# Kernel optimization log

Measured on AMD Instinct MI355X. Metric: run time of the kernel, lower is better.

## Reference

```python
import jax, jax.numpy as jnp
import numpy as np
import math

D_MODEL = 1024
N_HEADS = 16
D_HEAD = D_MODEL // N_HEADS


def setup_inputs() -> dict:
    key = jax.random.key(0)
    k_x, k_wqkv, k_bqkv, k_wp, k_bp = jax.random.split(key, 5)
    B, T = 2, 2048
    s = 1.0 / math.sqrt(D_MODEL)
    return {
        "x": jax.random.normal(k_x, (B, T, D_MODEL), dtype=jnp.float32),
        "W_qkv": jax.random.uniform(k_wqkv, (D_MODEL, 3 * D_MODEL), minval=-s, maxval=s, dtype=jnp.float32),
        "b_qkv": jax.random.uniform(k_bqkv, (3 * D_MODEL,), minval=-s, maxval=s, dtype=jnp.float32),
        "W_proj": jax.random.uniform(k_wp, (D_MODEL, D_MODEL), minval=-s, maxval=s, dtype=jnp.float32),
        "b_proj": jax.random.uniform(k_bp, (D_MODEL,), minval=-s, maxval=s, dtype=jnp.float32),
    }


def reference(x, W_qkv, b_qkv, W_proj, b_proj):
    B, T, C = x.shape
    qkv = x @ W_qkv + b_qkv                      # [B,T,3C]
    qkv = qkv.reshape(B, T, 3, N_HEADS, D_HEAD)
    qkv = jnp.transpose(qkv, (2, 0, 3, 1, 4))     # [3,B,H,T,dh]
    q, k, v = qkv[0], qkv[1], qkv[2]
    scale = math.sqrt(D_HEAD)
    attn = jnp.einsum('bhqd,bhkd->bhqk', q, k) / scale  # [B,H,T,T]
    causal = jnp.tril(jnp.ones((T, T), dtype=bool))
    attn = jnp.where(causal, attn, -jnp.inf)
    attn = jax.nn.softmax(attn, axis=-1)
    out = jnp.einsum('bhqk,bhkd->bhqd', attn, v)  # [B,H,T,dh]
    out = jnp.transpose(out, (0, 2, 1, 3)).reshape(B, T, C)
    return out @ W_proj + b_proj
```

## Files before the change

### kernel.cpp

```cpp
#include <hip/hip_runtime.h>

#define B_    2
#define T_    2048
#define C_    1024
#define H_    16
#define DH_   64
#define M_    (B_ * T_)
#define NQKV  (3 * C_)

typedef __bf16 bf16;
typedef __bf16 bf16x2 __attribute__((ext_vector_type(2)));
typedef __bf16 bf16x4 __attribute__((ext_vector_type(4)));
typedef __bf16 bf16x8 __attribute__((ext_vector_type(8)));
typedef float  f32x4  __attribute__((ext_vector_type(4)));
typedef float  f32x16 __attribute__((ext_vector_type(16)));
typedef unsigned u32x4 __attribute__((ext_vector_type(4)));

__device__ __forceinline__ void async16(const void* g, void* l) {
  __builtin_amdgcn_global_load_lds(
      (const __attribute__((address_space(1))) void*)g,
      (__attribute__((address_space(3))) void*)l, 16, 0, 0);
}

__device__ __forceinline__ unsigned pk(float a, float b) {
  bf16x2 t; t[0] = (bf16)a; t[1] = (bf16)b;
  return __builtin_bit_cast(unsigned, t);
}

__global__ __launch_bounds__(256) void prep_k(
    const float* __restrict__ x, bf16* __restrict__ xbf,
    const float* __restrict__ Wqkv, bf16* __restrict__ wqkvT,
    const float* __restrict__ Wproj, bf16* __restrict__ wprojT) {
  __shared__ float tile[32][33];
  const int bid = blockIdx.x;
  if (bid < 4096) {
    const int i = (bid * 256 + threadIdx.x) * 4;
    float4 v = *(const float4*)(x + i);
    bf16x4 o;
    o[0] = (bf16)v.x; o[1] = (bf16)v.y; o[2] = (bf16)v.z; o[3] = (bf16)v.w;
    *(bf16x4*)(xbf + i) = o;
    return;
  }
  const float* in; bf16* out; int R, C, cb, rb;
  if (bid < 4096 + 3072) {
    const int b = bid - 4096;
    in = Wqkv; out = wqkvT; R = 1024; C = 3072; cb = b % 96; rb = b / 96;
  } else {
    const int b = bid - 7168;
    in = Wproj; out = wprojT; R = 1024; C = 1024; cb = b & 31; rb = b >> 5;
  }
  const int c0 = cb * 32, r0 = rb * 32;
  const int tx = threadIdx.x & 31, ty = threadIdx.x >> 5;
#pragma unroll
  for (int j = 0; j < 4; j++)
    tile[ty + j * 8][tx] = in[(size_t)(r0 + ty + j * 8) * C + c0 + tx];
  __syncthreads();
#pragma unroll
  for (int j = 0; j < 4; j++)
    out[(size_t)(c0 + ty + j * 8) * R + r0 + tx] = (bf16)tile[tx][ty + j * 8];
}

template <int EPI, int BM, int BN>
__global__ __launch_bounds__(256) void gemm_k(
    const bf16* __restrict__ A, const bf16* __restrict__ Bt,
    const float* __restrict__ bias, float* __restrict__ outF,
    bf16* __restrict__ qb, bf16* __restrict__ kb, bf16* __restrict__ vtb) {
  constexpr int K = 1024;
  constexpr int MI = BM / 32;
  constexpr int NJ = BN / 32;
  __shared__ alignas(16) bf16 As[BM * 64];
  __shared__ alignas(16) bf16 Bs[BN * 64];
  const int tid = threadIdx.x;
  const int lane = tid & 63, wv = tid >> 6;
  const int l15 = lane & 15, quad = lane >> 4;
  const int wm = (wv >> 1) * (BM / 2), wn = (wv & 1) * (BN / 2);
  const int m0 = blockIdx.x * BM, n0 = blockIdx.y * BN;

  f32x4 acc[MI][NJ] = {};

  const int srow = tid >> 3;
  const int sgb = ((tid & 7) ^ (srow & 7)) * 8;
  const bf16* ga = A + (size_t)(m0 + srow) * K + sgb;
  const bf16* gb = Bt + (size_t)(n0 + srow) * K + sgb;
  const int swz = l15 & 7;

  for (int it = 0; it < K / 64; ++it) {
    const int k0 = it * 64;
#pragma unroll
    for (int c = 0; c < BM / 32; c++)
      async16(ga + k0 + (size_t)(c * 32) * K, As + tid * 8 + c * 2048);
#pragma unroll
    for (int c = 0; c < BN / 32; c++)
      async16(gb + k0 + (size_t)(c * 32) * K, Bs + tid * 8 + c * 2048);
    __syncthreads();
    bf16x8 af[2][MI], bfr[2][NJ];
#pragma unroll
    for (int kk = 0; kk < 2; kk++) {
#pragma unroll
      for (int i = 0; i < MI; i++)
        af[kk][i] = *(const bf16x8*)(As + (wm + i * 16 + l15) * 64 +
                                     (((kk * 4 + quad) ^ swz) << 3));
#pragma unroll
      for (int j = 0; j < NJ; j++)
        bfr[kk][j] = *(const bf16x8*)(Bs + (wn + j * 16 + l15) * 64 +
                                      (((kk * 4 + quad) ^ swz) << 3));
    }
#pragma unroll
    for (int kk = 0; kk < 2; kk++)
#pragma unroll
      for (int i = 0; i < MI; i++)
#pragma unroll
        for (int j = 0; j < NJ; j++)
          acc[i][j] = __builtin_amdgcn_mfma_f32_16x16x32_bf16(
              af[kk][i], bfr[kk][j], acc[i][j], 0, 0, 0);
    __syncthreads();
  }

#pragma unroll
  for (int i = 0; i < MI; i++) {
#pragma unroll
    for (int j = 0; j < NJ; j++) {
      const int gcol = n0 + wn + j * 16 + l15;
      const float bv = bias[gcol];
      const int trow = m0 + wm + i * 16 + quad * 4;
      if constexpr (EPI == 0) {
        const int which = gcol >> 10;
        const int hn = gcol & 1023;
        const int h = hn >> 6, d = hn & 63;
        const int bb = trow >> 11, t = trow & 2047;
        const int head = bb * 16 + h;
        if (which == 0) {
#pragma unroll
          for (int r = 0; r < 4; r++)
            qb[head * 131072 + (t + r) * 64 + d] =
                (bf16)((acc[i][j][r] + bv) * 0.1803368801f);
        } else if (which == 1) {
#pragma unroll
          for (int r = 0; r < 4; r++)
            kb[head * 131072 + (t + r) * 64 + d] = (bf16)(acc[i][j][r] + bv);
        } else {
          bf16x4 pv;
#pragma unroll
          for (int r = 0; r < 4; r++) pv[r] = (bf16)(acc[i][j][r] + bv);
          *(bf16x4*)(vtb + head * 131072 + d * 2048 + t) = pv;
        }
      } else {
#pragma unroll
        for (int r = 0; r < 4; r++)
          outF[(size_t)(trow + r) * 1024 + gcol] = acc[i][j][r] + bv;
      }
    }
  }
}

__global__ __launch_bounds__(512, 4) void attn_k(const bf16* __restrict__ Q,
                                                 const bf16* __restrict__ K,
                                                 const bf16* __restrict__ Vt,
                                                 bf16* __restrict__ O) {
  __shared__ alignas(16) bf16 Ks[2][128 * 64];
  __shared__ alignas(16) bf16 Vs[2][64 * 128];
  const int tid = threadIdx.x, lane = tid & 63, wv = tid >> 6;
  const int l31 = lane & 31, hi = lane >> 5;
  const int qs = wv & 3, halfw = wv >> 2;

  const int b = blockIdx.x;
  const int sH = b >> 8, i = b & 255;
  const int bh = (i & 7) | (((i >> 3) & 3) << 3);
  const int x = i >> 5;
  const int qJ = sH ? (15 - x) : x;
  const int q0 = qJ * 128;
  const int nIter = qJ + 1;

  const bf16* Qb = Q + (size_t)bh * 131072;
  const bf16* Kb = K + (size_t)bh * 131072;
  const bf16* Vb = Vt + (size_t)bh * 131072;

  const int krow = tid >> 3;
  const int kg = (tid & 7) ^ (krow & 7);
  const bf16* gk = Kb + krow * 64 + kg * 8;
  const int vrow = tid >> 4;
  const int vg = (tid & 15) ^ (vrow & 15);
  const bf16* gv = Vb + vrow * 2048 + vg * 8;

  const int swzk = l31 & 7;
  const int swzv = l31 & 15;
  const int bb = bh >> 4, h = bh & 15;

  const int q = q0 + qs * 32 + l31;
  bf16x8 aq[4];
#pragma unroll
  for (int ds = 0; ds < 4; ds++)
    aq[ds] = *(const bf16x8*)(Qb + q * 64 + ds * 16 + hi * 8);

  f32x16 o0 = {}, o1 = {};
  float m = -3.0e38f, lsum = 0.f;

#pragma unroll
  for (int c = 0; c < 2; c++) {
    async16(gk + c * (64 * 64), &Ks[0][tid * 8 + c * 4096]);
    async16(gv + c * (32 * 2048), &Vs[0][tid * 8 + c * 4096]);
  }

  for (int it = 0; it < nIter; ++it) {
    const int cur = it & 1;
    __syncthreads();
    if (it + 1 < nIter) {
      const int kt1 = (it + 1) * 128;
#pragma unroll
      for (int c = 0; c < 2; c++) {
        async16(gk + kt1 * 64 + c * (64 * 64), &Ks[cur ^ 1][tid * 8 + c * 4096]);
        async16(gv + kt1 + c * (32 * 2048), &Vs[cur ^ 1][tid * 8 + c * 4096]);
      }
    }
    const bf16* Kc = Ks[cur];
    const bf16* Vc = Vs[cur];

    f32x16 s[2] = {};
    __builtin_amdgcn_s_setprio(1);
#pragma unroll
    for (int nf = 0; nf < 2; nf++) {
      const int row = halfw * 64 + nf * 32 + l31;
#pragma unroll
      for (int ds = 0; ds < 4; ds++) {
        bf16x8 kf = *(const bf16x8*)(Kc + row * 64 + (((ds * 2 + hi) ^ swzk) << 3));
        s[nf] = __builtin_amdgcn_mfma_f32_32x32x16_bf16(kf, aq[ds], s[nf], 0, 0, 0);
      }
    }
    __builtin_amdgcn_s_setprio(0);

    if (it == nIter - 1) {
#pragma unroll
      for (int nf = 0; nf < 2; nf++)
#pragma unroll
        for (int r = 0; r < 16; r++) {
          const int kt = it * 128 + halfw * 64 + nf * 32 +
                         (r & 3) + 8 * (r >> 2) + 4 * hi;
          if (kt > q) s[nf][r] = -3.0e38f;
        }
    }

    float red[8];
#pragma unroll
    for (int r = 0; r < 8; r++)
      red[r] = fmaxf(fmaxf(s[0][r], s[0][r + 8]), fmaxf(s[1][r], s[1][r + 8]));
#pragma unroll
    for (int st = 4; st >= 1; st >>= 1)
#pragma unroll
      for (int r = 0; r < 4; r++)
        if (r < st) red[r] = fmaxf(red[r], red[r + st]);
    float mx = red[0];
    mx = fmaxf(mx, __shfl_xor(mx, 32));
    if (!__all(mx - m <= 8.0f)) {
      const float mnew = fmaxf(m, mx);
      const float alpha = __builtin_amdgcn_exp2f(m - mnew);
      m = mnew; lsum *= alpha;
#pragma unroll
      for (int r = 0; r < 16; r++) { o0[r] *= alpha; o1[r] *= alpha; }
    }
    float tsp[4] = {0.f, 0.f, 0.f, 0.f};
    unsigned w[2][8];
#pragma unroll
    for (int nf = 0; nf < 2; nf++)
#pragma unroll
      for (int k = 0; k < 8; k++) {
        const float pa = __builtin_amdgcn_exp2f(s[nf][2 * k] - m);
        const float pc = __builtin_amdgcn_exp2f(s[nf][2 * k + 1] - m);
        tsp[k & 3] += pa + pc;
        w[nf][k] = pk(pa, pc);
      }
    float ts = (tsp[0] + tsp[1]) + (tsp[2] + tsp[3]);
    ts += __shfl_xor(ts, 32);
    lsum += ts;

    __builtin_amdgcn_s_setprio(1);
#pragma unroll
    for (int nf = 0; nf < 2; nf++) {
#pragma unroll
      for (int hh = 0; hh < 2; hh++) {
        const unsigned w0 = w[nf][hh * 4 + 0], w1 = w[nf][hh * 4 + 1];
        const unsigned w2 = w[nf][hh * 4 + 2], w3 = w[nf][hh * 4 + 3];
        const unsigned rx = (unsigned)__shfl_xor((int)(hi ? w0 : w2), 32);
        const unsigned ry = (unsigned)__shfl_xor((int)(hi ? w1 : w3), 32);
        u32x4 pw;
        pw[0] = hi ? rx : w0;
        pw[1] = hi ? ry : w1;
        pw[2] = hi ? w2 : rx;
        pw[3] = hi ? w3 : ry;
        const bf16x8 pb = __builtin_bit_cast(bf16x8, pw);
        const int c = halfw * 4 + nf * 2 + hh;
        const bf16x8 vf0 = *(const bf16x8*)(Vc + l31 * 128 +
                                            (((c * 2 + hi) ^ swzv) << 3));
        o0 = __builtin_amdgcn_mfma_f32_32x32x16_bf16(vf0, pb, o0, 0, 0, 0);
        const bf16x8 vf1 = *(const bf16x8*)(Vc + (32 + l31) * 128 +
                                            (((c * 2 + hi) ^ swzv) << 3));
        o1 = __builtin_amdgcn_mfma_f32_32x32x16_bf16(vf1, pb, o1, 0, 0, 0);
      }
    }
    __builtin_amdgcn_s_setprio(0);
  }

  __syncthreads();
  float* oX = (float*)Vs;
  float* mX = (float*)Ks;
  const int slot = qs * 64 + lane;
  if (halfw == 1) {
#pragma unroll
    for (int r = 0; r < 16; r++) {
      oX[r * 256 + slot] = o0[r];
      oX[(16 + r) * 256 + slot] = o1[r];
    }
    mX[slot] = m;
    mX[256 + slot] = lsum;
  }
  __syncthreads();
  if (halfw == 0) {
    const float mB = mX[slot], lB = mX[256 + slot];
    const float m12 = fmaxf(m, mB);
    const float aA = __builtin_amdgcn_exp2f(m - m12);
    const float aB = __builtin_amdgcn_exp2f(mB - m12);
    const float inv = 1.0f / (lsum * aA + lB * aB);
    bf16* Op = O + (size_t)(bb * 2048 + q) * 1024 + h * 64;
#pragma unroll
    for (int g = 0; g < 4; g++) {
      bf16x4 v0, v1;
#pragma unroll
      for (int k2 = 0; k2 < 4; k2++) {
        const int r = g * 4 + k2;
        v0[k2] = (bf16)((o0[r] * aA + oX[r * 256 + slot] * aB) * inv);
        v1[k2] = (bf16)((o1[r] * aA + oX[(16 + r) * 256 + slot] * aB) * inv);
      }
      *(bf16x4*)(Op + g * 8 + hi * 4) = v0;
      *(bf16x4*)(Op + 32 + g * 8 + hi * 4) = v1;
    }
  }
}

extern "C" void kernel_launch(void* const* d_in, const int* in_sizes, int n_in,
                              void* d_out, int out_size, void* d_ws, size_t ws_size,
                              hipStream_t stream) {
  const float* x     = (const float*)d_in[0];
  const float* Wqkv  = (const float*)d_in[1];
  const float* bqkv  = (const float*)d_in[2];
  const float* Wproj = (const float*)d_in[3];
  const float* bproj = (const float*)d_in[4];
  float* out = (float*)d_out;

  char* p = (char*)d_ws;
  bf16* xbf    = (bf16*)p; p += (size_t)M_ * C_ * 2;
  bf16* wqkvT  = (bf16*)p; p += (size_t)NQKV * C_ * 2;
  bf16* wprojT = (bf16*)p; p += (size_t)C_ * C_ * 2;
  bf16* Qb     = (bf16*)p; p += (size_t)M_ * C_ * 2;
  bf16* Kb     = (bf16*)p; p += (size_t)M_ * C_ * 2;
  bf16* Vtb    = (bf16*)p; p += (size_t)M_ * C_ * 2;
  bf16* AO     = (bf16*)p;

  prep_k<<<8192, 256, 0, stream>>>(x, xbf, Wqkv, wqkvT, Wproj, wprojT);

  gemm_k<0, 128, 128><<<dim3(M_ / 128, NQKV / 128), 256, 0, stream>>>(
      xbf, wqkvT, bqkv, nullptr, Qb, Kb, Vtb);

  attn_k<<<512, 512, 0, stream>>>(Qb, Kb, Vtb, AO);

  gemm_k<1, 64, 64><<<dim3(M_ / 64, C_ / 64), 256, 0, stream>>>(
      AO, wprojT, bproj, out, nullptr, nullptr, nullptr);
}
```

Before: 165.8 us.

## Split attention key tiles across four waves with smaller query blocks

The attention kernel now handles 64-query blocks, giving twice as many workgroups. Each of 4 wave groups processes a 32-key slice of each 128-key tile, and the partial softmax states are merged by a two-level LDS tree reduction at the end. K is single-buffered with an extra barrier per iteration, and Q is reloaded from global memory each iteration instead of held in registers. The launch bound moves to 6 to raise occupancy, at the cost of more barriers, repeated Q loads and a longer cross-wave merge.

```diff
diff --git a/kernel.cpp b/kernel.cpp
--- a/kernel.cpp
+++ b/kernel.cpp
@@ -153,23 +153,23 @@
   }
 }
 
-__global__ __launch_bounds__(512, 4) void attn_k(const bf16* __restrict__ Q,
+__global__ __launch_bounds__(512, 6) void attn_k(const bf16* __restrict__ Q,
                                                  const bf16* __restrict__ K,
                                                  const bf16* __restrict__ Vt,
                                                  bf16* __restrict__ O) {
-  __shared__ alignas(16) bf16 Ks[2][128 * 64];
+  __shared__ alignas(16) bf16 Ks[128 * 64];
   __shared__ alignas(16) bf16 Vs[2][64 * 128];
   const int tid = threadIdx.x, lane = tid & 63, wv = tid >> 6;
   const int l31 = lane & 31, hi = lane >> 5;
-  const int qs = wv & 3, halfw = wv >> 2;
+  const int qs = wv & 1, ktq = wv >> 1;
 
   const int b = blockIdx.x;
-  const int sH = b >> 8, i = b & 255;
+  const int sH = b >> 9, i = b & 511;
   const int bh = (i & 7) | (((i >> 3) & 3) << 3);
   const int x = i >> 5;
-  const int qJ = sH ? (15 - x) : x;
-  const int q0 = qJ * 128;
-  const int nIter = qJ + 1;
+  const int qJ = sH ? (31 - x) : x;
+  const int q0 = qJ * 64;
+  const int nIter = (qJ >> 1) + 1;
 
   const bf16* Qb = Q + (size_t)bh * 131072;
   const bf16* Kb = K + (size_t)bh * 131072;
@@ -187,68 +187,58 @@
   const int bb = bh >> 4, h = bh & 15;
 
   const int q = q0 + qs * 32 + l31;
-  bf16x8 aq[4];
-#pragma unroll
-  for (int ds = 0; ds < 4; ds++)
-    aq[ds] = *(const bf16x8*)(Qb + q * 64 + ds * 16 + hi * 8);
+  const int krow_rd = ktq * 32 + l31;
 
   f32x16 o0 = {}, o1 = {};
   float m = -3.0e38f, lsum = 0.f;
 
-#pragma unroll
-  for (int c = 0; c < 2; c++) {
-    async16(gk + c * (64 * 64), &Ks[0][tid * 8 + c * 4096]);
-    async16(gv + c * (32 * 2048), &Vs[0][tid * 8 + c * 4096]);
-  }
+  async16(gk, &Ks[tid * 8]);
+  async16(gk + 4096, &Ks[tid * 8 + 4096]);
+  async16(gv, &Vs[0][tid * 8]);
+  async16(gv + 32 * 2048, &Vs[0][tid * 8 + 4096]);
 
   for (int it = 0; it < nIter; ++it) {
-    const int cur = it & 1;
     __syncthreads();
     if (it + 1 < nIter) {
       const int kt1 = (it + 1) * 128;
-#pragma unroll
-      for (int c = 0; c < 2; c++) {
-        async16(gk + kt1 * 64 + c * (64 * 64), &Ks[cur ^ 1][tid * 8 + c * 4096]);
-        async16(gv + kt1 + c * (32 * 2048), &Vs[cur ^ 1][tid * 8 + c * 4096]);
+      async16(gv + kt1, &Vs[(it + 1) & 1][tid * 8]);
+      async16(gv + kt1 + 32 * 2048, &Vs[(it + 1) & 1][tid * 8 + 4096]);
+    }
+    bf16x8 aq[4];
+#pragma unroll
+    for (int ds = 0; ds < 4; ds++)
+      aq[ds] = *(const bf16x8*)(Qb + q * 64 + ds * 16 + hi * 8);
+
+    f32x16 s = {};
+    __builtin_amdgcn_s_setprio(1);
+#pragma unroll
+    for (int ds = 0; ds < 4; ds++) {
+      bf16x8 kf = *(const bf16x8*)(Ks + krow_rd * 64 +
+                                   (((ds * 2 + hi) ^ swzk) << 3));
+      s = __builtin_amdgcn_mfma_f32_32x32x16_bf16(kf, aq[ds], s, 0, 0, 0);
+    }
+    __builtin_amdgcn_s_setprio(0);
+
+    __syncthreads();
+    if (it + 1 < nIter) {
+      const int kt1 = (it + 1) * 128;
+      async16(gk + kt1 * 64, &Ks[tid * 8]);
+      async16(gk + kt1 * 64 + 4096, &Ks[tid * 8 + 4096]);
+    }
+
+    if (it == nIter - 1) {
+#pragma unroll
+      for (int r = 0; r < 16; r++) {
+        const int kt = it * 128 + ktq * 32 + (r & 3) + 8 * (r >> 2) + 4 * hi;
+        if (kt > q) s[r] = -3.0e38f;
       }
     }
-    const bf16* Kc = Ks[cur];
-    const bf16* Vc = Vs[cur];
-
-    f32x16 s[2] = {};
-    __builtin_amdgcn_s_setprio(1);
-#pragma unroll
-    for (int nf = 0; nf < 2; nf++) {
-      const int row = halfw * 64 + nf * 32 + l31;
-#pragma unroll
-      for (int ds = 0; ds < 4; ds++) {
-        bf16x8 kf = *(const bf16x8*)(Kc + row * 64 + (((ds * 2 + hi) ^ swzk) << 3));
-        s[nf] = __builtin_amdgcn_mfma_f32_32x32x16_bf16(kf, aq[ds], s[nf], 0, 0, 0);
-      }
-    }
-    __builtin_amdgcn_s_setprio(0);
-
-    if (it == nIter - 1) {
-#pragma unroll
-      for (int nf = 0; nf < 2; nf++)
-#pragma unroll
-        for (int r = 0; r < 16; r++) {
-          const int kt = it * 128 + halfw * 64 + nf * 32 +
-                         (r & 3) + 8 * (r >> 2) + 4 * hi;
-          if (kt > q) s[nf][r] = -3.0e38f;
-        }
-    }
-
-    float red[8];
-#pragma unroll
-    for (int r = 0; r < 8; r++)
-      red[r] = fmaxf(fmaxf(s[0][r], s[0][r + 8]), fmaxf(s[1][r], s[1][r + 8]));
-#pragma unroll
-    for (int st = 4; st >= 1; st >>= 1)
-#pragma unroll
-      for (int r = 0; r < 4; r++)
-        if (r < st) red[r] = fmaxf(red[r], red[r + st]);
-    float mx = red[0];
+
+    float red[4];
+#pragma unroll
+    for (int r = 0; r < 4; r++)
+      red[r] = fmaxf(fmaxf(s[r], s[r + 4]), fmaxf(s[r + 8], s[r + 12]));
+    float mx = fmaxf(fmaxf(red[0], red[2]), fmaxf(red[1], red[3]));
     mx = fmaxf(mx, __shfl_xor(mx, 32));
     if (!__all(mx - m <= 8.0f)) {
       const float mnew = fmaxf(m, mx);
@@ -258,43 +248,39 @@
       for (int r = 0; r < 16; r++) { o0[r] *= alpha; o1[r] *= alpha; }
     }
     float tsp[4] = {0.f, 0.f, 0.f, 0.f};
-    unsigned w[2][8];
-#pragma unroll
-    for (int nf = 0; nf < 2; nf++)
-#pragma unroll
-      for (int k = 0; k < 8; k++) {
-        const float pa = __builtin_amdgcn_exp2f(s[nf][2 * k] - m);
-        const float pc = __builtin_amdgcn_exp2f(s[nf][2 * k + 1] - m);
-        tsp[k & 3] += pa + pc;
-        w[nf][k] = pk(pa, pc);
-      }
+    unsigned w[8];
+#pragma unroll
+    for (int k = 0; k < 8; k++) {
+      const float pa = __builtin_amdgcn_exp2f(s[2 * k] - m);
+      const float pc = __builtin_amdgcn_exp2f(s[2 * k + 1] - m);
+      tsp[k & 3] += pa + pc;
+      w[k] = pk(pa, pc);
+    }
     float ts = (tsp[0] + tsp[1]) + (tsp[2] + tsp[3]);
     ts += __shfl_xor(ts, 32);
     lsum += ts;
 
+    const bf16* Vc = Vs[it & 1];
     __builtin_amdgcn_s_setprio(1);
 #pragma unroll
-    for (int nf = 0; nf < 2; nf++) {
-#pragma unroll
-      for (int hh = 0; hh < 2; hh++) {
-        const unsigned w0 = w[nf][hh * 4 + 0], w1 = w[nf][hh * 4 + 1];
-        const unsigned w2 = w[nf][hh * 4 + 2], w3 = w[nf][hh * 4 + 3];
-        const unsigned rx = (unsigned)__shfl_xor((int)(hi ? w0 : w2), 32);
-        const unsigned ry = (unsigned)__shfl_xor((int)(hi ? w1 : w3), 32);
-        u32x4 pw;
-        pw[0] = hi ? rx : w0;
-        pw[1] = hi ? ry : w1;
-        pw[2] = hi ? w2 : rx;
-        pw[3] = hi ? w3 : ry;
-        const bf16x8 pb = __builtin_bit_cast(bf16x8, pw);
-        const int c = halfw * 4 + nf * 2 + hh;
-        const bf16x8 vf0 = *(const bf16x8*)(Vc + l31 * 128 +
-                                            (((c * 2 + hi) ^ swzv) << 3));
-        o0 = __builtin_amdgcn_mfma_f32_32x32x16_bf16(vf0, pb, o0, 0, 0, 0);
-        const bf16x8 vf1 = *(const bf16x8*)(Vc + (32 + l31) * 128 +
-                                            (((c * 2 + hi) ^ swzv) << 3));
-        o1 = __builtin_amdgcn_mfma_f32_32x32x16_bf16(vf1, pb, o1, 0, 0, 0);
-      }
+    for (int hh = 0; hh < 2; hh++) {
+      const unsigned w0 = w[hh * 4 + 0], w1 = w[hh * 4 + 1];
+      const unsigned w2 = w[hh * 4 + 2], w3 = w[hh * 4 + 3];
+      const unsigned rx = (unsigned)__shfl_xor((int)(hi ? w0 : w2), 32);
+      const unsigned ry = (unsigned)__shfl_xor((int)(hi ? w1 : w3), 32);
+      u32x4 pw;
+      pw[0] = hi ? rx : w0;
+      pw[1] = hi ? ry : w1;
+      pw[2] = hi ? w2 : rx;
+      pw[3] = hi ? w3 : ry;
+      const bf16x8 pb = __builtin_bit_cast(bf16x8, pw);
+      const int c = ktq * 2 + hh;
+      const bf16x8 vf0 = *(const bf16x8*)(Vc + l31 * 128 +
+                                          (((c * 2 + hi) ^ swzv) << 3));
+      o0 = __builtin_amdgcn_mfma_f32_32x32x16_bf16(vf0, pb, o0, 0, 0, 0);
+      const bf16x8 vf1 = *(const bf16x8*)(Vc + (32 + l31) * 128 +
+                                          (((c * 2 + hi) ^ swzv) << 3));
+      o1 = __builtin_amdgcn_mfma_f32_32x32x16_bf16(vf1, pb, o1, 0, 0, 0);
     }
     __builtin_amdgcn_s_setprio(0);
   }
@@ -302,19 +288,43 @@
   __syncthreads();
   float* oX = (float*)Vs;
   float* mX = (float*)Ks;
-  const int slot = qs * 64 + lane;
-  if (halfw == 1) {
+  const int slot = qs * 2 + (ktq >> 1);
+  if (ktq & 1) {
 #pragma unroll
     for (int r = 0; r < 16; r++) {
-      oX[r * 256 + slot] = o0[r];
-      oX[(16 + r) * 256 + slot] = o1[r];
-    }
-    mX[slot] = m;
-    mX[256 + slot] = lsum;
-  }
-  __syncthreads();
-  if (halfw == 0) {
-    const float mB = mX[slot], lB = mX[256 + slot];
+      oX[slot * 2048 + r * 64 + lane] = o0[r];
+      oX[slot * 2048 + (16 + r) * 64 + lane] = o1[r];
+    }
+    mX[slot * 128 + lane] = m;
+    mX[slot * 128 + 64 + lane] = lsum;
+  }
+  __syncthreads();
+  if (!(ktq & 1)) {
+    const float mB = mX[slot * 128 + lane], lB = mX[slot * 128 + 64 + lane];
+    const float m12 = fmaxf(m, mB);
+    const float aA = __builtin_amdgcn_exp2f(m - m12);
+    const float aB = __builtin_amdgcn_exp2f(mB - m12);
+    lsum = lsum * aA + lB * aB;
+#pragma unroll
+    for (int r = 0; r < 16; r++) {
+      o0[r] = o0[r] * aA + oX[slot * 2048 + r * 64 + lane] * aB;
+      o1[r] = o1[r] * aA + oX[slot * 2048 + (16 + r) * 64 + lane] * aB;
+    }
+    m = m12;
+  }
+  __syncthreads();
+  if (ktq == 2) {
+#pragma unroll
+    for (int r = 0; r < 16; r++) {
+      oX[qs * 2048 + r * 64 + lane] = o0[r];
+      oX[qs * 2048 + (16 + r) * 64 + lane] = o1[r];
+    }
+    mX[qs * 128 + lane] = m;
+    mX[qs * 128 + 64 + lane] = lsum;
+  }
+  __syncthreads();
+  if (ktq == 0) {
+    const float mB = mX[qs * 128 + lane], lB = mX[qs * 128 + 64 + lane];
     const float m12 = fmaxf(m, mB);
     const float aA = __builtin_amdgcn_exp2f(m - m12);
     const float aB = __builtin_amdgcn_exp2f(mB - m12);
@@ -326,8 +336,8 @@
 #pragma unroll
       for (int k2 = 0; k2 < 4; k2++) {
         const int r = g * 4 + k2;
-        v0[k2] = (bf16)((o0[r] * aA + oX[r * 256 + slot] * aB) * inv);
-        v1[k2] = (bf16)((o1[r] * aA + oX[(16 + r) * 256 + slot] * aB) * inv);
+        v0[k2] = (bf16)((o0[r] * aA + oX[qs * 2048 + r * 64 + lane] * aB) * inv);
+        v1[k2] = (bf16)((o1[r] * aA + oX[qs * 2048 + (16 + r) * 64 + lane] * aB) * inv);
       }
       *(bf16x4*)(Op + g * 8 + hi * 4) = v0;
       *(bf16x4*)(Op + 32 + g * 8 + hi * 4) = v1;
@@ -359,7 +369,7 @@
   gemm_k<0, 128, 128><<<dim3(M_ / 128, NQKV / 128), 256, 0, stream>>>(
       xbf, wqkvT, bqkv, nullptr, Qb, Kb, Vtb);
 
-  attn_k<<<512, 512, 0, stream>>>(Qb, Kb, Vtb, AO);
+  attn_k<<<1024, 512, 0, stream>>>(Qb, Kb, Vtb, AO);
 
   gemm_k<1, 64, 64><<<dim3(M_ / 64, C_ / 64), 256, 0, stream>>>(
       AO, wprojT, bproj, out, nullptr, nullptr, nullptr);
```

Result: slower. 184.3 us (+11.2%).
